# Kernel tuning notes

Hardware: AMD Instinct MI355X
Metric: run time of the kernel (lower is better)

Reference implementation:

```python
import jax, jax.numpy as jnp
import numpy as np

N, E, F_IN, C = 50000, 800000, 128, 300
NEG_SLOPE = 0.2  # PyG GATv2Conv default negative_slope


def setup_inputs() -> dict:
    key = jax.random.key(0)
    ks = jax.random.split(key, 10)
    x = jax.random.normal(ks[0], (N, F_IN), dtype=jnp.float32)
    edge_index = jax.random.randint(ks[1], (2, E), 0, N, dtype=jnp.int64)
    s_in = np.float32(1.0 / np.sqrt(F_IN))
    s_c = np.float32(1.0 / np.sqrt(C))
    Wl = jax.random.normal(ks[2], (F_IN, C), dtype=jnp.float32) * s_in
    bl = jnp.zeros((C,), jnp.float32)
    Wr = jax.random.normal(ks[3], (F_IN, C), dtype=jnp.float32) * s_in
    br = jnp.zeros((C,), jnp.float32)
    att = jax.random.normal(ks[4], (C,), dtype=jnp.float32) * s_c
    bias = jnp.zeros((C,), jnp.float32)
    lw = jax.random.normal(ks[5], (C, 1), dtype=jnp.float32) * s_c
    lb = jnp.zeros((1,), jnp.float32)
    return {"x": x, "edge_index": edge_index, "Wl": Wl, "bl": bl,
            "Wr": Wr, "br": br, "att": att, "bias": bias, "lw": lw, "lb": lb}


def reference(x, edge_index, Wl, bl, Wr, br, att, bias, lw, lb):
    n = x.shape[0]
    # GATv2: separate source/target linear transforms
    xl = x @ Wl + bl  # [N, C] (source / message features)
    xr = x @ Wr + br  # [N, C] (target features)
    # add self loops (PyG default add_self_loops=True)
    loops = jnp.arange(n, dtype=edge_index.dtype)
    src = jnp.concatenate([edge_index[0], loops])  # [E+N]
    dst = jnp.concatenate([edge_index[1], loops])  # [E+N]
    # GATv2 attention logit: a^T LeakyReLU(xl_j + xr_i)
    e = jax.nn.leaky_relu(xl[src] + xr[dst], NEG_SLOPE) @ att  # [E+N]
    # segment softmax over incoming edges of each target node
    m = jax.ops.segment_max(e, dst, num_segments=n)
    ex = jnp.exp(e - m[dst])
    denom = jax.ops.segment_sum(ex, dst, num_segments=n)
    alpha = ex / denom[dst]  # [E+N]
    # weighted scatter-aggregation of source messages + conv bias
    out = jax.ops.segment_sum(xl[src] * alpha[:, None], dst, num_segments=n) + bias
    h = jax.nn.relu(out)          # torch.relu
    # F.dropout in eval mode is identity (reference is inference math)
    return jax.nn.sigmoid(h @ lw + lb)  # [N, 1]
```

## Files before the change

kernel.cpp:

```cpp
#include <hip/hip_runtime.h>
#include <hip/hip_fp16.h>

#define F_IN 128
#define C_DIM 300
#define NEG_SLOPE 0.2f
#define NCT  40
#define CH   8
#define NPB  256

typedef _Float16 half8 __attribute__((ext_vector_type(8)));
typedef _Float16 half4 __attribute__((ext_vector_type(4)));
typedef _Float16 h2    __attribute__((ext_vector_type(2)));
typedef float    f32x4 __attribute__((ext_vector_type(4)));
typedef float    f32x2 __attribute__((ext_vector_type(2)));

__device__ inline h2 as_h2(unsigned u) { union { unsigned u; h2 h; } c; c.u = u; return c.h; }
__device__ inline unsigned as_u(h2 h)  { union { unsigned u; h2 h; } c; c.h = h; return c.u; }
__device__ inline f32x2 upv(unsigned u) {
    h2 h = as_h2(u);
    f32x2 r; r.x = (float)h.x; r.y = (float)h.y; return r;
}

#if __has_builtin(__builtin_amdgcn_fdot2)
__device__ inline float fdot2w(h2 a, h2 b, float c) {
    return __builtin_amdgcn_fdot2(a, b, c, false);
}
#else
__device__ inline float fdot2w(h2 a, h2 b, float c) {
    return fmaf((float)a.y, (float)b.y, fmaf((float)a.x, (float)b.x, c));
}
#endif

__global__ __launch_bounds__(256) void convert_w(
    const float* __restrict__ Wl, const float* __restrict__ Wr,
    _Float16* __restrict__ Bp)
{
    int idx = blockIdx.x * 256 + threadIdx.x;
    if (idx >= 640 * F_IN) return;
    int nn = idx % 640;
    int k  = idx / 640;
    float v = 0.f;
    if (nn < 300)                   v = Wl[k * C_DIM + nn];
    else if (nn >= 304 && nn < 604) v = Wr[k * C_DIM + (nn - 304)];
    int ct = nn >> 4, n16 = nn & 15;
    int kr = k & 31,  ks  = k >> 5;
    int lane = ((kr >> 3) << 4) | n16;
    int j = k & 7;
    Bp[((((ct * 4 + ks) * 64) + lane) << 3) | j] = (_Float16)v;
}

__global__ __launch_bounds__(256) void gemm_xlxr(
    const float* __restrict__ x, const _Float16* __restrict__ Bp,
    const float* __restrict__ bl, const float* __restrict__ br,
    _Float16* __restrict__ xlh, _Float16* __restrict__ xrh, int n)
{
    __shared__ __align__(16) _Float16 xs[64][136];
    const int rb0 = blockIdx.x * 64;
    const int t   = threadIdx.x;

    #pragma unroll
    for (int i = 0; i < 8; ++i) {
        int flat = (i * 256 + t) * 4;
        int r = flat >> 7;
        int k = flat & 127;
        int gr = rb0 + r;
        if (gr >= n) gr = n - 1;
        float4 v = *reinterpret_cast<const float4*>(x + (size_t)gr * F_IN + k);
        half4 h = { (_Float16)v.x, (_Float16)v.y, (_Float16)v.z, (_Float16)v.w };
        *reinterpret_cast<half4*>(&xs[r][k]) = h;
    }
    __syncthreads();

    const int w    = t >> 6;
    const int lane = t & 63;
    const int m    = lane & 15;
    const int quad = lane >> 4;

    half8 a[4];
    #pragma unroll
    for (int ks = 0; ks < 4; ++ks)
        a[ks] = *reinterpret_cast<const half8*>(&xs[w * 16 + m][ks * 32 + quad * 8]);

    const int rbase = rb0 + w * 16 + quad * 4;

    #pragma unroll 4
    for (int ct = 0; ct < NCT; ++ct) {
        f32x4 acc = {0.f, 0.f, 0.f, 0.f};
        #pragma unroll
        for (int ks = 0; ks < 4; ++ks) {
            half8 b = *reinterpret_cast<const half8*>(
                Bp + (((size_t)(ct * 4 + ks) * 64 + lane) << 3));
            acc = __builtin_amdgcn_mfma_f32_16x16x32_f16(a[ks], b, acc, 0, 0, 0);
        }
        int col = ct * 16 + m;
        int isL = (col < 300);
        int isR = (col >= 304 && col < 604);
        if (isL | isR) {
            float bv = isL ? bl[col] : br[col - 304];
            _Float16* tab = isL ? (xlh + col) : (xrh + (col - 304));
            #pragma unroll
            for (int reg = 0; reg < 4; ++reg) {
                int row = rbase + reg;
                if (row < n)
                    tab[(size_t)row * C_DIM] = (_Float16)(acc[reg] + bv);
            }
        }
    }
}

__global__ __launch_bounds__(256) void bucket_count(
    const int* __restrict__ dst, unsigned* __restrict__ bcnt, int nE, int chunk)
{
    __shared__ unsigned cnt[256];
    const int b = blockIdx.x, t = threadIdx.x;
    cnt[t] = 0;
    __syncthreads();
    const int lo = b * chunk;
    const int hi = min(nE, lo + chunk);
    for (int i = lo + t; i < hi; i += 256)
        atomicAdd(&cnt[dst[i] >> 8], 1u);
    __syncthreads();
    bcnt[t * NPB + b] = cnt[t];
}

__global__ __launch_bounds__(256) void scan_part(
    const unsigned* __restrict__ counts, unsigned* __restrict__ bsum, int n)
{
    __shared__ unsigned s[256];
    const int t = threadIdx.x;
    const int base = blockIdx.x * 1024 + t * 4;
    unsigned v = 0;
    #pragma unroll
    for (int i = 0; i < 4; ++i) {
        int idx = base + i;
        if (idx < n) v += counts[idx];
    }
    s[t] = v;
    __syncthreads();
    for (int off = 128; off > 0; off >>= 1) {
        if (t < off) s[t] += s[t + off];
        __syncthreads();
    }
    if (t == 0) bsum[blockIdx.x] = s[0];
}

__global__ __launch_bounds__(256) void scan_final(
    const unsigned* __restrict__ counts, const unsigned* __restrict__ bsum,
    unsigned* __restrict__ offs, int n, int nblk)
{
    __shared__ unsigned s[256];
    __shared__ unsigned sbase;
    const int t = threadIdx.x;
    if (t < 64) {
        unsigned v64 = (t < nblk) ? bsum[t] : 0u;
        unsigned inc = v64;
        #pragma unroll
        for (int off = 1; off < 64; off <<= 1) {
            unsigned u = __shfl_up(inc, off);
            if (t >= off) inc += u;
        }
        if (t == (int)blockIdx.x) sbase = inc - v64;
        if (blockIdx.x == gridDim.x - 1 && t == 63) offs[n] = inc;
    }
    const int base = blockIdx.x * 1024 + t * 4;
    unsigned c[4];
    unsigned v = 0;
    #pragma unroll
    for (int i = 0; i < 4; ++i) {
        int idx = base + i;
        c[i] = (idx < n) ? counts[idx] : 0u;
        v += c[i];
    }
    s[t] = v;
    __syncthreads();
    for (int off = 1; off < 256; off <<= 1) {
        unsigned u = (t >= off) ? s[t - off] : 0u;
        __syncthreads();
        if (t >= off) s[t] += u;
        __syncthreads();
    }
    unsigned run = sbase + s[t] - v;
    #pragma unroll
    for (int i = 0; i < 4; ++i) {
        int idx = base + i;
        if (idx < n) {
            offs[idx] = run;
            run += c[i];
        }
    }
}

__global__ __launch_bounds__(256) void partition_edges(
    const int* __restrict__ src, const int* __restrict__ dst,
    const unsigned* __restrict__ boff,
    unsigned* __restrict__ ebuf, int nE, int chunk)
{
    __shared__ unsigned cur[256];
    const int b = blockIdx.x, t = threadIdx.x;
    cur[t] = boff[t * NPB + b];
    __syncthreads();
    const int lo = b * chunk;
    const int hi = min(nE, lo + chunk);
    for (int i = lo + t; i < hi; i += 256) {
        int d  = dst[i];
        int sv = src[i];
        unsigned p = atomicAdd(&cur[d >> 8], 1u);
        ebuf[p] = (unsigned)sv | ((unsigned)(d & 255) << 16);
    }
}

__global__ __launch_bounds__(256) void bucket_csr(
    const unsigned* __restrict__ ebuf, const unsigned* __restrict__ boff,
    unsigned* __restrict__ offs, int* __restrict__ csr_src, int n, int nE, int nb)
{
    __shared__ unsigned cnt[256];
    __shared__ unsigned s[256];
    __shared__ unsigned cur[256];
    const int bk = blockIdx.x;
    const int t  = threadIdx.x;
    const unsigned bstart = boff[(unsigned)bk * NPB];
    const unsigned bend   = boff[(unsigned)(bk + 1) * NPB];
    cnt[t] = 0;
    __syncthreads();
    for (unsigned i = bstart + t; i < bend; i += 256)
        atomicAdd(&cnt[(ebuf[i] >> 16) & 255], 1u);
    __syncthreads();
    unsigned v = cnt[t];
    s[t] = v;
    __syncthreads();
    for (int off = 1; off < 256; off <<= 1) {
        unsigned u = (t >= off) ? s[t - off] : 0u;
        __syncthreads();
        if (t >= off) s[t] += u;
        __syncthreads();
    }
    const unsigned excl = s[t] - v;
    const int node = (bk << 8) + t;
    if (node <= n) offs[node] = bstart + excl;
    if (t == 0 && bk == nb - 1 && (n & 255) == 0) offs[n] = (unsigned)nE;
    cur[t] = bstart + excl;
    __syncthreads();
    for (unsigned i = bstart + t; i < bend; i += 256) {
        unsigned e = ebuf[i];
        unsigned p = atomicAdd(&cur[(e >> 16) & 255], 1u);
        csr_src[p] = (int)(e & 0xFFFFu);
    }
}

__global__ __launch_bounds__(256) void gat_gather(
    const int* __restrict__ csr_src, const unsigned* __restrict__ offs,
    const _Float16* __restrict__ xlh, const _Float16* __restrict__ xrh,
    const float* __restrict__ att, const float* __restrict__ bias,
    const float* __restrict__ lw, const float* __restrict__ lb,
    float* __restrict__ y, int n)
{
    __shared__ __align__(16) float lds[4 * 560];
    float* part = lds + (threadIdx.x >> 6) * 560;

    const int wid  = (blockIdx.x * blockDim.x + threadIdx.x) >> 6;
    const int lane = threadIdx.x & 63;
    if (wid >= n) return;

    const int l2   = 2 * lane;
    const bool has2 = (lane < 22);
    const int t8   = lane & 7;
    const int o    = lane >> 3;
    const int byteoff = lane * 4;

    const _Float16* xrrow = xrh + (size_t)wid * C_DIM;
    h2 xr0 = *(const h2*)(xrrow + l2);
    h2 xr1 = *(const h2*)(xrrow + 128 + l2);
    h2 xr2 = {(_Float16)0, (_Float16)0};
    if (has2) xr2 = *(const h2*)(xrrow + 256 + l2);

    h2 a06[3], a04[3];
    #pragma unroll
    for (int k = 0; k < 3; ++k) {
        int c = 128 * k + l2;
        float ax = (c < C_DIM) ? att[c] : 0.f;
        float ay = (c + 1 < C_DIM) ? att[c + 1] : 0.f;
        a06[k].x = (_Float16)(0.6f * ax); a06[k].y = (_Float16)(0.6f * ay);
        a04[k].x = (_Float16)(0.4f * ax); a04[k].y = (_Float16)(0.4f * ay);
    }

    f32x2 acc2[3] = {{0.f, 0.f}, {0.f, 0.f}, {0.f, 0.f}};
    float den_l = 0.f;

    const unsigned start = offs[wid];
    const int totalE = (int)(offs[wid + 1] - start) + 1;
    const char* basep = (const char*)xlh;

    int idv = wid;
    {
        int k = lane;
        if (lane < CH && k > 0 && k < totalE) idv = csr_src[start + k - 1];
    }

    for (int base = 0; base < totalE; base += CH) {
        int rowb = idv * (C_DIM * 2);
        int ro[CH];
        #pragma unroll
        for (int tt = 0; tt < CH; ++tt) ro[tt] = __shfl(rowb, tt);

        unsigned pk0[CH], pk1[CH], pk2[CH];
        #pragma unroll
        for (int tt = 0; tt < CH; ++tt) {
            const char* p = basep + ro[tt] + byteoff;
            pk0[tt] = *(const unsigned*)(p);
            pk1[tt] = *(const unsigned*)(p + 256);
            pk2[tt] = 0u;
        }
        if (has2) {
            #pragma unroll
            for (int tt = 0; tt < CH; ++tt)
                pk2[tt] = *(const unsigned*)(basep + ro[tt] + byteoff + 512);
        }

        idv = wid;
        {
            int k = base + CH + lane;
            if (lane < CH && k > 0 && k < totalE) idv = csr_src[start + k - 1];
        }

        #pragma unroll
        for (int tt = 0; tt < CH; ++tt) {
            h2 z0 = as_h2(pk0[tt]) + xr0;
            h2 z1 = as_h2(pk1[tt]) + xr1;
            h2 z2 = as_h2(pk2[tt]) + xr2;
            float p = fdot2w(z0, a06[0], 0.f);
            p = fdot2w(as_h2(as_u(z0) & 0x7FFF7FFFu), a04[0], p);
            p = fdot2w(z1, a06[1], p);
            p = fdot2w(as_h2(as_u(z1) & 0x7FFF7FFFu), a04[1], p);
            p = fdot2w(z2, a06[2], p);
            p = fdot2w(as_h2(as_u(z2) & 0x7FFF7FFFu), a04[2], p);
            part[tt * 68 + lane] = p;
        }

        float wgt;
        {
            const int oo = (o + t8) & 7;
            const float* rp = part + t8 * 68 + oo * 8;
            float4 s0 = *(const float4*)(rp + 0);
            float4 s1 = *(const float4*)(rp + 4);
            float e = ((s0.x + s0.y) + (s0.z + s0.w)) + ((s1.x + s1.y) + (s1.z + s1.w));
            e += __shfl_xor(e, 8);
            e += __shfl_xor(e, 16);
            e += __shfl_xor(e, 32);
            bool valid = (base + t8) < totalE;
            wgt = valid ? __expf(fminf(e, 60.f)) : 0.f;
        }

        den_l += wgt;

        _Float16 wh = (_Float16)wgt;
        h2 wpair = {wh, wh};
        unsigned wbits = as_u(wpair);
        h2 hacc0 = {(_Float16)0, (_Float16)0};
        h2 hacc1 = {(_Float16)0, (_Float16)0};
        h2 hacc2 = {(_Float16)0, (_Float16)0};
        #pragma unroll
        for (int tt = 0; tt < CH; ++tt) {
            h2 wt2 = as_h2(__shfl(wbits, tt));
            hacc0 += wt2 * as_h2(pk0[tt]);
            hacc1 += wt2 * as_h2(pk1[tt]);
            hacc2 += wt2 * as_h2(pk2[tt]);
        }
        acc2[0] += upv(as_u(hacc0));
        acc2[1] += upv(as_u(hacc1));
        acc2[2] += upv(as_u(hacc2));
    }

    float den = den_l;
    den += __shfl_xor(den, 1);
    den += __shfl_xor(den, 2);
    den += __shfl_xor(den, 4);

    const float invd = 1.f / den;
    float dot = 0.f;
    #pragma unroll
    for (int k = 0; k < 3; ++k) {
        #pragma unroll
        for (int j = 0; j < 2; ++j) {
            int c = 128 * k + l2 + j;
            float b = (c < C_DIM) ? bias[c] : 0.f;
            float l = (c < C_DIM) ? lw[c] : 0.f;
            float a = (j == 0) ? acc2[k].x : acc2[k].y;
            float h = fmaf(a, invd, b);
            h = h > 0.f ? h : 0.f;
            dot = fmaf(h, l, dot);
        }
    }
    #pragma unroll
    for (int off = 32; off; off >>= 1) dot += __shfl_xor(dot, off);
    if (lane == 0) y[wid] = 1.f / (1.f + __expf(-(dot + lb[0])));
}

extern "C" void kernel_launch(void* const* d_in, const int* in_sizes, int n_in,
                              void* d_out, int out_size, void* d_ws, size_t ws_size,
                              hipStream_t stream)
{
    const float* x    = (const float*)d_in[0];
    const int*   ei   = (const int*)d_in[1];
    const float* Wl   = (const float*)d_in[2];
    const float* bl   = (const float*)d_in[3];
    const float* Wr   = (const float*)d_in[4];
    const float* br   = (const float*)d_in[5];
    const float* att  = (const float*)d_in[6];
    const float* bias = (const float*)d_in[7];
    const float* lw   = (const float*)d_in[8];
    const float* lb   = (const float*)d_in[9];
    float* y = (float*)d_out;

    const int n  = in_sizes[0] / F_IN;
    const int nE = in_sizes[1] / 2;
    const int* src_arr = ei;
    const int* dst_arr = ei + nE;

    const int NB    = (n + 255) >> 8;
    const int chunk = (nE + NPB - 1) / NPB;
    const int M     = 256 * NPB;
    const int nblkM = (M + 1023) / 1024;

    _Float16* xlh      = (_Float16*)d_ws;
    _Float16* xrh      = xlh + (size_t)n * C_DIM;
    _Float16* Bp       = xrh + (size_t)n * C_DIM;
    unsigned* bcnt     = (unsigned*)(Bp + NCT * 4 * 64 * 8);
    unsigned* boff     = bcnt + M;
    unsigned* offs     = boff + (M + 1);
    unsigned* bsum     = offs + (n + 1);
    int*      csr_src  = (int*)(bsum + 64);
    unsigned* ebuf     = (unsigned*)(csr_src + nE);

    convert_w<<<(640 * F_IN + 255) / 256, 256, 0, stream>>>(Wl, Wr, Bp);

    bucket_count<<<NPB, 256, 0, stream>>>(dst_arr, bcnt, nE, chunk);
    scan_part<<<nblkM, 256, 0, stream>>>(bcnt, bsum, M);
    scan_final<<<nblkM, 256, 0, stream>>>(bcnt, bsum, boff, M, nblkM);
    partition_edges<<<NPB, 256, 0, stream>>>(src_arr, dst_arr, boff, ebuf, nE, chunk);
    bucket_csr<<<NB, 256, 0, stream>>>(ebuf, boff, offs, csr_src, n, nE, NB);

    gemm_xlxr<<<(n + 63) / 64, 256, 0, stream>>>(x, Bp, bl, br, xlh, xrh, n);

    gat_gather<<<(n + 3) / 4, 256, 0, stream>>>(csr_src, offs, xlh, xrh, att, bias, lw, lb, y, n);
}
```

Baseline: 243.8 us.

## Double GEMM row tile, trim padded column tiles, vectorize edge loads

The xl/xr GEMM now processes 128 rows per block with two MFMA row tiles per wave, so each B fragment loaded from global memory is reused twice. The padded column tile count drops from 40 to 38, skipping tiles that were all padding. The bucket_count and partition_edges kernels read dst/src as int4 vectors instead of scalars to cut load instructions. In exchange the GEMM holds more registers and LDS per block and launches half as many blocks. The int4 reinterpret of the dst pointer at ei+nE assumes 16-byte alignment, which holds here only because nE is a multiple of 4.

```diff
diff --git a/kernel.cpp b/kernel.cpp
--- a/kernel.cpp
+++ b/kernel.cpp
@@ -4,9 +4,10 @@
 #define F_IN 128
 #define C_DIM 300
 #define NEG_SLOPE 0.2f
-#define NCT  40
+#define NCT  38
 #define CH   8
 #define NPB  256
+#define RB   128
 
 typedef _Float16 half8 __attribute__((ext_vector_type(8)));
 typedef _Float16 half4 __attribute__((ext_vector_type(4)));
@@ -36,9 +37,9 @@
     _Float16* __restrict__ Bp)
 {
     int idx = blockIdx.x * 256 + threadIdx.x;
-    if (idx >= 640 * F_IN) return;
-    int nn = idx % 640;
-    int k  = idx / 640;
+    if (idx >= 608 * F_IN) return;
+    int nn = idx % 608;
+    int k  = idx / 608;
     float v = 0.f;
     if (nn < 300)                   v = Wl[k * C_DIM + nn];
     else if (nn >= 304 && nn < 604) v = Wr[k * C_DIM + (nn - 304)];
@@ -54,12 +55,12 @@
     const float* __restrict__ bl, const float* __restrict__ br,
     _Float16* __restrict__ xlh, _Float16* __restrict__ xrh, int n)
 {
-    __shared__ __align__(16) _Float16 xs[64][136];
-    const int rb0 = blockIdx.x * 64;
+    __shared__ __align__(16) _Float16 xs[RB][136];
+    const int rb0 = blockIdx.x * RB;
     const int t   = threadIdx.x;
 
     #pragma unroll
-    for (int i = 0; i < 8; ++i) {
+    for (int i = 0; i < 16; ++i) {
         int flat = (i * 256 + t) * 4;
         int r = flat >> 7;
         int k = flat & 127;
@@ -76,21 +77,25 @@
     const int m    = lane & 15;
     const int quad = lane >> 4;
 
-    half8 a[4];
-    #pragma unroll
-    for (int ks = 0; ks < 4; ++ks)
-        a[ks] = *reinterpret_cast<const half8*>(&xs[w * 16 + m][ks * 32 + quad * 8]);
-
-    const int rbase = rb0 + w * 16 + quad * 4;
-
-    #pragma unroll 4
+    half8 a[2][4];
+    #pragma unroll
+    for (int mt = 0; mt < 2; ++mt)
+        #pragma unroll
+        for (int ks = 0; ks < 4; ++ks)
+            a[mt][ks] = *reinterpret_cast<const half8*>(
+                &xs[w * 32 + mt * 16 + m][ks * 32 + quad * 8]);
+
+    const int rbase0 = rb0 + w * 32 + quad * 4;
+
+    #pragma unroll 2
     for (int ct = 0; ct < NCT; ++ct) {
-        f32x4 acc = {0.f, 0.f, 0.f, 0.f};
+        f32x4 acc[2] = {{0.f,0.f,0.f,0.f},{0.f,0.f,0.f,0.f}};
         #pragma unroll
         for (int ks = 0; ks < 4; ++ks) {
             half8 b = *reinterpret_cast<const half8*>(
                 Bp + (((size_t)(ct * 4 + ks) * 64 + lane) << 3));
-            acc = __builtin_amdgcn_mfma_f32_16x16x32_f16(a[ks], b, acc, 0, 0, 0);
+            acc[0] = __builtin_amdgcn_mfma_f32_16x16x32_f16(a[0][ks], b, acc[0], 0, 0, 0);
+            acc[1] = __builtin_amdgcn_mfma_f32_16x16x32_f16(a[1][ks], b, acc[1], 0, 0, 0);
         }
         int col = ct * 16 + m;
         int isL = (col < 300);
@@ -99,26 +104,43 @@
             float bv = isL ? bl[col] : br[col - 304];
             _Float16* tab = isL ? (xlh + col) : (xrh + (col - 304));
             #pragma unroll
-            for (int reg = 0; reg < 4; ++reg) {
-                int row = rbase + reg;
-                if (row < n)
-                    tab[(size_t)row * C_DIM] = (_Float16)(acc[reg] + bv);
+            for (int mt = 0; mt < 2; ++mt) {
+                #pragma unroll
+                for (int reg = 0; reg < 4; ++reg) {
+                    int row = rbase0 + mt * 16 + reg;
+                    if (row < n)
+                        tab[(size_t)row * C_DIM] = (_Float16)(acc[mt][reg] + bv);
+                }
             }
         }
     }
 }
 
 __global__ __launch_bounds__(256) void bucket_count(
-    const int* __restrict__ dst, unsigned* __restrict__ bcnt, int nE, int chunk)
+    const int* __restrict__ dst, unsigned* __restrict__ bcnt, int nE, int chunk4)
 {
     __shared__ unsigned cnt[256];
     const int b = blockIdx.x, t = threadIdx.x;
     cnt[t] = 0;
     __syncthreads();
-    const int lo = b * chunk;
-    const int hi = min(nE, lo + chunk);
-    for (int i = lo + t; i < hi; i += 256)
-        atomicAdd(&cnt[dst[i] >> 8], 1u);
+    const int4* dst4 = reinterpret_cast<const int4*>(dst);
+    const int total4 = (nE + 3) >> 2;
+    const int lo = b * chunk4;
+    const int hi = min(total4, lo + chunk4);
+    for (int i = lo + t; i < hi; i += 256) {
+        int4 d = dst4[i];
+        int e = i * 4;
+        if (e + 3 < nE) {
+            atomicAdd(&cnt[d.x >> 8], 1u);
+            atomicAdd(&cnt[d.y >> 8], 1u);
+            atomicAdd(&cnt[d.z >> 8], 1u);
+            atomicAdd(&cnt[d.w >> 8], 1u);
+        } else {
+            if (e < nE)     atomicAdd(&cnt[d.x >> 8], 1u);
+            if (e + 1 < nE) atomicAdd(&cnt[d.y >> 8], 1u);
+            if (e + 2 < nE) atomicAdd(&cnt[d.z >> 8], 1u);
+        }
+    }
     __syncthreads();
     bcnt[t * NPB + b] = cnt[t];
 }
@@ -193,19 +215,30 @@
 __global__ __launch_bounds__(256) void partition_edges(
     const int* __restrict__ src, const int* __restrict__ dst,
     const unsigned* __restrict__ boff,
-    unsigned* __restrict__ ebuf, int nE, int chunk)
+    unsigned* __restrict__ ebuf, int nE, int chunk4)
 {
     __shared__ unsigned cur[256];
     const int b = blockIdx.x, t = threadIdx.x;
     cur[t] = boff[t * NPB + b];
     __syncthreads();
-    const int lo = b * chunk;
-    const int hi = min(nE, lo + chunk);
+    const int4* dst4 = reinterpret_cast<const int4*>(dst);
+    const int4* src4 = reinterpret_cast<const int4*>(src);
+    const int total4 = (nE + 3) >> 2;
+    const int lo = b * chunk4;
+    const int hi = min(total4, lo + chunk4);
     for (int i = lo + t; i < hi; i += 256) {
-        int d  = dst[i];
-        int sv = src[i];
-        unsigned p = atomicAdd(&cur[d >> 8], 1u);
-        ebuf[p] = (unsigned)sv | ((unsigned)(d & 255) << 16);
+        int4 d = dst4[i];
+        int4 s = src4[i];
+        int e = i * 4;
+        int dv[4] = {d.x, d.y, d.z, d.w};
+        int sv[4] = {s.x, s.y, s.z, s.w};
+        #pragma unroll
+        for (int j = 0; j < 4; ++j) {
+            if (e + j < nE) {
+                unsigned p = atomicAdd(&cur[dv[j] >> 8], 1u);
+                ebuf[p] = (unsigned)sv[j] | ((unsigned)(dv[j] & 255) << 16);
+            }
+        }
     }
 }
 
@@ -416,10 +449,11 @@
     const int* src_arr = ei;
     const int* dst_arr = ei + nE;
 
-    const int NB    = (n + 255) >> 8;
-    const int chunk = (nE + NPB - 1) / NPB;
-    const int M     = 256 * NPB;
-    const int nblkM = (M + 1023) / 1024;
+    const int NB     = (n + 255) >> 8;
+    const int total4 = (nE + 3) >> 2;
+    const int chunk4 = (total4 + NPB - 1) / NPB;
+    const int M      = 256 * NPB;
+    const int nblkM  = (M + 1023) / 1024;
 
     _Float16* xlh      = (_Float16*)d_ws;
     _Float16* xrh      = xlh + (size_t)n * C_DIM;
@@ -431,15 +465,15 @@
     int*      csr_src  = (int*)(bsum + 64);
     unsigned* ebuf     = (unsigned*)(csr_src + nE);
 
-    convert_w<<<(640 * F_IN + 255) / 256, 256, 0, stream>>>(Wl, Wr, Bp);
-
-    bucket_count<<<NPB, 256, 0, stream>>>(dst_arr, bcnt, nE, chunk);
+    convert_w<<<(608 * F_IN + 255) / 256, 256, 0, stream>>>(Wl, Wr, Bp);
+
+    bucket_count<<<NPB, 256, 0, stream>>>(dst_arr, bcnt, nE, chunk4);
     scan_part<<<nblkM, 256, 0, stream>>>(bcnt, bsum, M);
     scan_final<<<nblkM, 256, 0, stream>>>(bcnt, bsum, boff, M, nblkM);
-    partition_edges<<<NPB, 256, 0, stream>>>(src_arr, dst_arr, boff, ebuf, nE, chunk);
+    partition_edges<<<NPB, 256, 0, stream>>>(src_arr, dst_arr, boff, ebuf, nE, chunk4);
     bucket_csr<<<NB, 256, 0, stream>>>(ebuf, boff, offs, csr_src, n, nE, NB);
 
-    gemm_xlxr<<<(n + 63) / 64, 256, 0, stream>>>(x, Bp, bl, br, xlh, xrh, n);
+    gemm_xlxr<<<(n + RB - 1) / RB, 256, 0, stream>>>(x, Bp, bl, br, xlh, xrh, n);
 
     gat_gather<<<(n + 3) / 4, 256, 0, stream>>>(csr_src, offs, xlh, xrh, att, bias, lw, lb, y, n);
 }
```

New measurement: 255.8 us. 4.9% more time.
